# Kernel optimization log

Hardware: AMD Instinct MI355X
Metric: run time of the kernel (lower is better)

Reference implementation:

```python
import jax, jax.numpy as jnp
import numpy as np

ITERATION = 10

def setup_inputs() -> dict:
    key = jax.random.key(0)
    k1, k2, k3 = jax.random.split(key, 3)
    a_inter = jax.random.normal(k1, (8, 64, 64, 32, 32), dtype=jnp.float32)
    logits = jax.random.normal(k2, (8, 64), dtype=jnp.float32)
    W = jax.random.normal(k3, (1, 64, 64), dtype=jnp.float32)
    return {"a_inter": a_inter, "logits": logits, "W": W}


def reference(a_inter, logits, W):
    N = W.shape[1]  # num_nodes
    B = a_inter.shape[0]
    # feats: [B, N, C*H*W]
    feats = a_inter[:, :, :N, :, :].reshape(B, N, -1)
    # expand logits [B, N] -> [B, N, N] (unsqueeze(1).expand in torch)
    logits0 = jnp.broadcast_to(logits[:, None, :], (B, N, N))

    feats_norm = jnp.linalg.norm(feats, ord=2, axis=2, keepdims=True)  # [B, N, 1]
    pairwise_norm = feats_norm @ jnp.swapaxes(feats_norm, 1, 2)        # [B, N, N]
    pairwise_dot = feats @ jnp.swapaxes(feats, 1, 2)                   # [B, N, N]
    pairwise_sim = pairwise_dot / (pairwise_norm + 1e-6)
    W_sym = (W + jnp.swapaxes(W, 1, 2)) / 2.0
    pairwise_potential = pairwise_sim * W_sym                          # [B, N, N]

    unary_potential = logits0

    def body(i, l):
        probs = jnp.swapaxes(jax.nn.sigmoid(l), 1, 2)  # [B, N, N]
        # probs*pp - (1-probs)*pp == (2*probs - 1)*pp
        pp_E = jnp.sum((2.0 * probs - 1.0) * pairwise_potential, axis=2, keepdims=True)
        return unary_potential + pp_E

    logits_out = jax.lax.fori_loop(0, ITERATION, body, logits0)
    return logits_out.mean(axis=1)  # [B, N]
```

## Files before the change

### kernel.cpp

```cpp
#include <hip/hip_runtime.h>
#include <math.h>

#define BATCH 8
#define NN 64
#define DD 65536
#define BPB 64
#define NBLK (BATCH * BPB)
#define KC (DD / BPB)
#define KW (KC / 4)
#define KSTEPS (KW / 32)
#define NTRI 10
#define PSZ (NTRI * 256)

typedef float  floatx4 __attribute__((ext_vector_type(4)));
typedef __bf16 bf16x8  __attribute__((ext_vector_type(8)));

static __device__ __forceinline__ bf16x8 cvt8(float4 lo, float4 hi) {
    const unsigned sel = 0x07060302u;
    union { unsigned u[4]; bf16x8 v; } r;
    r.u[0] = __builtin_amdgcn_perm(__float_as_uint(lo.y), __float_as_uint(lo.x), sel);
    r.u[1] = __builtin_amdgcn_perm(__float_as_uint(lo.w), __float_as_uint(lo.z), sel);
    r.u[2] = __builtin_amdgcn_perm(__float_as_uint(hi.y), __float_as_uint(hi.x), sel);
    r.u[3] = __builtin_amdgcn_perm(__float_as_uint(hi.w), __float_as_uint(hi.z), sel);
    return r.v;
}

__global__ __launch_bounds__(256, 3) void gram_partial_kernel(const float* __restrict__ a,
                                                              float* __restrict__ part) {
    __shared__ __align__(16) float red[3][NTRI][64][4];

    const int bid = blockIdx.x;
    const int b = bid >> 6;
    const int c = bid & (BPB - 1);

    const int tid  = threadIdx.x;
    const int w    = tid >> 6;
    const int lane = tid & 63;
    const int m    = lane & 15;
    const int q    = lane >> 4;

    const float* base = a + (size_t)b * NN * DD + (size_t)c * KC + (size_t)w * KW
                          + (size_t)m * DD + q * 8;
    const float* p0 = base;
    const float* p1 = base + (size_t)16 * DD;
    const float* p2 = base + (size_t)32 * DD;
    const float* p3 = base + (size_t)48 * DD;

    floatx4 acc[NTRI];
    #pragma unroll
    for (int i = 0; i < NTRI; ++i) acc[i] = (floatx4)0.0f;

    float4 A0, A1, A2, A3, A4, A5, A6, A7;
    float4 B0, B1, B2, B3, B4, B5, B6, B7;

#define LOADSET(R0,R1,R2,R3,R4,R5,R6,R7, o)                                \
    R0 = *(const float4*)(p0 + (o));  R1 = *(const float4*)(p0 + (o) + 4); \
    R2 = *(const float4*)(p1 + (o));  R3 = *(const float4*)(p1 + (o) + 4); \
    R4 = *(const float4*)(p2 + (o));  R5 = *(const float4*)(p2 + (o) + 4); \
    R6 = *(const float4*)(p3 + (o));  R7 = *(const float4*)(p3 + (o) + 4);

#define MFMASET(R0,R1,R2,R3,R4,R5,R6,R7)                                   \
    {                                                                      \
        bf16x8 f0 = cvt8(R0, R1);                                          \
        bf16x8 f1 = cvt8(R2, R3);                                          \
        bf16x8 f2 = cvt8(R4, R5);                                          \
        bf16x8 f3 = cvt8(R6, R7);                                          \
        acc[0] = __builtin_amdgcn_mfma_f32_16x16x32_bf16(f0, f0, acc[0], 0, 0, 0); \
        acc[1] = __builtin_amdgcn_mfma_f32_16x16x32_bf16(f0, f1, acc[1], 0, 0, 0); \
        acc[2] = __builtin_amdgcn_mfma_f32_16x16x32_bf16(f0, f2, acc[2], 0, 0, 0); \
        acc[3] = __builtin_amdgcn_mfma_f32_16x16x32_bf16(f0, f3, acc[3], 0, 0, 0); \
        acc[4] = __builtin_amdgcn_mfma_f32_16x16x32_bf16(f1, f1, acc[4], 0, 0, 0); \
        acc[5] = __builtin_amdgcn_mfma_f32_16x16x32_bf16(f1, f2, acc[5], 0, 0, 0); \
        acc[6] = __builtin_amdgcn_mfma_f32_16x16x32_bf16(f1, f3, acc[6], 0, 0, 0); \
        acc[7] = __builtin_amdgcn_mfma_f32_16x16x32_bf16(f2, f2, acc[7], 0, 0, 0); \
        acc[8] = __builtin_amdgcn_mfma_f32_16x16x32_bf16(f2, f3, acc[8], 0, 0, 0); \
        acc[9] = __builtin_amdgcn_mfma_f32_16x16x32_bf16(f3, f3, acc[9], 0, 0, 0); \
    }

    LOADSET(A0,A1,A2,A3,A4,A5,A6,A7, 0)
    #pragma unroll
    for (int s = 0; s < KSTEPS; s += 2) {
        LOADSET(B0,B1,B2,B3,B4,B5,B6,B7, (s + 1) * 32)
        MFMASET(A0,A1,A2,A3,A4,A5,A6,A7)
        if (s + 2 < KSTEPS) { LOADSET(A0,A1,A2,A3,A4,A5,A6,A7, (s + 2) * 32) }
        MFMASET(B0,B1,B2,B3,B4,B5,B6,B7)
    }
#undef LOADSET
#undef MFMASET

    if (w > 0) {
        #pragma unroll
        for (int t = 0; t < NTRI; ++t)
            *(floatx4*)&red[w - 1][t][lane][0] = acc[t];
    }
    __syncthreads();
    if (w == 0) {
        #pragma unroll
        for (int t = 0; t < NTRI; ++t) {
            floatx4 r0 = *(const floatx4*)&red[0][t][lane][0];
            floatx4 r1 = *(const floatx4*)&red[1][t][lane][0];
            floatx4 r2 = *(const floatx4*)&red[2][t][lane][0];
            acc[t] += (r0 + r1) + r2;
        }
        float* pg = part + (size_t)bid * PSZ;
        #pragma unroll
        for (int t = 0; t < NTRI; ++t) {
            float* tp = pg + t * 256 + m;
            #pragma unroll
            for (int r = 0; r < 4; ++r)
                tp[(q * 4 + r) * 16] = acc[t][r];
        }
    }
}

__global__ __launch_bounds__(128) void gram_reduce_kernel(const float* __restrict__ part,
                                                          float* __restrict__ gram) {
    const int gid = blockIdx.x * 128 + threadIdx.x;
    const int b   = gid >> 12;
    const int idx = gid & 4095;
    const int i   = idx >> 6;
    const int j   = idx & 63;
    const int ti  = i >> 4, tj = j >> 4;
    const int ib  = ti <= tj ? ti : tj;
    const int jb  = ti <= tj ? tj : ti;
    const int slot = ib * 4 - (ib * (ib - 1)) / 2 + (jb - ib);
    const int rr  = (ti <= tj) ? (i & 15) : (j & 15);
    const int cc  = (ti <= tj) ? (j & 15) : (i & 15);
    const int off = slot * 256 + rr * 16 + cc;
    const float* p = part + (size_t)b * BPB * PSZ + off;

    float s0 = 0.f, s1 = 0.f, s2 = 0.f, s3 = 0.f;
    #pragma unroll 4
    for (int c = 0; c < BPB; c += 4) {
        s0 += p[(size_t)(c + 0) * PSZ];
        s1 += p[(size_t)(c + 1) * PSZ];
        s2 += p[(size_t)(c + 2) * PSZ];
        s3 += p[(size_t)(c + 3) * PSZ];
    }
    gram[gid] = (s0 + s1) + (s2 + s3);
}

__global__ __launch_bounds__(256) void crf_kernel(const float* __restrict__ gram,
                                                  const float* __restrict__ logits,
                                                  const float* __restrict__ Wm,
                                                  float* __restrict__ out) {
    __shared__ float pp[NN][NN + 1];
    __shared__ float E[NN];
    __shared__ float nrm[NN];
    __shared__ float part[4 * NN];

    const int b  = blockIdx.x;
    const int tid = threadIdx.x;
    const int i  = tid & 63;
    const int jq = tid >> 6;
    const float* g = gram + b * NN * NN;

    if (jq == 0) nrm[i] = sqrtf(g[i * NN + i]);
    E[i] = 0.0f;
    __syncthreads();

    const float ni = nrm[i];
    for (int jj = 0; jj < 16; ++jj) {
        int j = jq * 16 + jj;
        float wsym = 0.5f * (Wm[i * NN + j] + Wm[j * NN + i]);
        pp[i][j] = g[i * NN + j] / (ni * nrm[j] + 1e-6f) * wsym;
    }
    const float li = logits[b * NN + i];
    __syncthreads();

    for (int it = 0; it < 10; ++it) {
        float acc = 0.0f;
        for (int jj = 0; jj < 16; ++jj) {
            int j = jq * 16 + jj;
            float t = li + E[j];
            float s = 1.0f / (1.0f + expf(-t));
            acc = fmaf(2.0f * s - 1.0f, pp[i][j], acc);
        }
        part[jq * NN + i] = acc;
        __syncthreads();
        if (jq == 0)
            E[i] = part[i] + part[NN + i] + part[2 * NN + i] + part[3 * NN + i];
        __syncthreads();
    }

    if (tid < 64) {
        float s = E[tid];
        for (int off = 32; off > 0; off >>= 1) s += __shfl_down(s, off);
        float meanE = __shfl(s, 0) * (1.0f / 64.0f);
        out[b * NN + tid] = logits[b * NN + tid] + meanE;
    }
}

extern "C" void kernel_launch(void* const* d_in, const int* in_sizes, int n_in,
                              void* d_out, int out_size, void* d_ws, size_t ws_size,
                              hipStream_t stream) {
    const float* a      = (const float*)d_in[0];
    const float* logits = (const float*)d_in[1];
    const float* Wm     = (const float*)d_in[2];
    float* out  = (float*)d_out;

    float* part = (float*)d_ws;
    float* gram = part + (size_t)NBLK * PSZ;

    gram_partial_kernel<<<NBLK, 256, 0, stream>>>(a, part);
    gram_reduce_kernel<<<(BATCH * NN * NN) / 128, 128, 0, stream>>>(part, gram);
    crf_kernel<<<BATCH, 256, 0, stream>>>(gram, logits, Wm, out);
}
```

Before: 217.8 us.

## Stage bf16-converted feature chunks through double-buffered LDS for coalesced loads

The gram partial kernel now has each thread load contiguous float4s across rows, convert them to bf16 and write them into a double-buffered padded LDS tile. Each wave then reads its MFMA fragments from shared memory instead of doing strided per-lane global loads. The aim is fully coalesced global reads and an overlap of the next chunk's load with the current MFMAs. In exchange it adds LDS traffic and a block-wide barrier per chunk, and fewer loads are kept in flight per thread than in the old register-pipelined loop.

After: 225.3 us. 1.03x slower.

```diff
diff --git a/kernel.cpp b/kernel.cpp
--- a/kernel.cpp
+++ b/kernel.cpp
@@ -7,27 +7,21 @@
 #define BPB 64
 #define NBLK (BATCH * BPB)
 #define KC (DD / BPB)
-#define KW (KC / 4)
-#define KSTEPS (KW / 32)
+#define CHUNK 128
+#define NCHUNK (KC / CHUNK)
+#define LROW 144
 #define NTRI 10
 #define PSZ (NTRI * 256)
 
 typedef float  floatx4 __attribute__((ext_vector_type(4)));
 typedef __bf16 bf16x8  __attribute__((ext_vector_type(8)));
 
-static __device__ __forceinline__ bf16x8 cvt8(float4 lo, float4 hi) {
-    const unsigned sel = 0x07060302u;
-    union { unsigned u[4]; bf16x8 v; } r;
-    r.u[0] = __builtin_amdgcn_perm(__float_as_uint(lo.y), __float_as_uint(lo.x), sel);
-    r.u[1] = __builtin_amdgcn_perm(__float_as_uint(lo.w), __float_as_uint(lo.z), sel);
-    r.u[2] = __builtin_amdgcn_perm(__float_as_uint(hi.y), __float_as_uint(hi.x), sel);
-    r.u[3] = __builtin_amdgcn_perm(__float_as_uint(hi.w), __float_as_uint(hi.z), sel);
-    return r.v;
-}
-
 __global__ __launch_bounds__(256, 3) void gram_partial_kernel(const float* __restrict__ a,
                                                               float* __restrict__ part) {
-    __shared__ __align__(16) float red[3][NTRI][64][4];
+    __shared__ __align__(16) union {
+        unsigned short st[2][64 * LROW];
+        float red[3][NTRI][64][4];
+    } sh;
 
     const int bid = blockIdx.x;
     const int b = bid >> 6;
@@ -39,68 +33,72 @@
     const int m    = lane & 15;
     const int q    = lane >> 4;
 
-    const float* base = a + (size_t)b * NN * DD + (size_t)c * KC + (size_t)w * KW
-                          + (size_t)m * DD + q * 8;
-    const float* p0 = base;
-    const float* p1 = base + (size_t)16 * DD;
-    const float* p2 = base + (size_t)32 * DD;
-    const float* p3 = base + (size_t)48 * DD;
+    const int r0 = tid >> 5;
+    const int kp = tid & 31;
+    const float* gbase = a + (size_t)b * NN * DD + (size_t)c * KC
+                           + (size_t)r0 * DD + kp * 4;
+    const int lbase = r0 * LROW + kp * 4;
+
+    const unsigned sel = 0x07060302u;
 
     floatx4 acc[NTRI];
     #pragma unroll
     for (int i = 0; i < NTRI; ++i) acc[i] = (floatx4)0.0f;
 
-    float4 A0, A1, A2, A3, A4, A5, A6, A7;
-    float4 B0, B1, B2, B3, B4, B5, B6, B7;
-
-#define LOADSET(R0,R1,R2,R3,R4,R5,R6,R7, o)                                \
-    R0 = *(const float4*)(p0 + (o));  R1 = *(const float4*)(p0 + (o) + 4); \
-    R2 = *(const float4*)(p1 + (o));  R3 = *(const float4*)(p1 + (o) + 4); \
-    R4 = *(const float4*)(p2 + (o));  R5 = *(const float4*)(p2 + (o) + 4); \
-    R6 = *(const float4*)(p3 + (o));  R7 = *(const float4*)(p3 + (o) + 4);
-
-#define MFMASET(R0,R1,R2,R3,R4,R5,R6,R7)                                   \
-    {                                                                      \
-        bf16x8 f0 = cvt8(R0, R1);                                          \
-        bf16x8 f1 = cvt8(R2, R3);                                          \
-        bf16x8 f2 = cvt8(R4, R5);                                          \
-        bf16x8 f3 = cvt8(R6, R7);                                          \
-        acc[0] = __builtin_amdgcn_mfma_f32_16x16x32_bf16(f0, f0, acc[0], 0, 0, 0); \
-        acc[1] = __builtin_amdgcn_mfma_f32_16x16x32_bf16(f0, f1, acc[1], 0, 0, 0); \
-        acc[2] = __builtin_amdgcn_mfma_f32_16x16x32_bf16(f0, f2, acc[2], 0, 0, 0); \
-        acc[3] = __builtin_amdgcn_mfma_f32_16x16x32_bf16(f0, f3, acc[3], 0, 0, 0); \
-        acc[4] = __builtin_amdgcn_mfma_f32_16x16x32_bf16(f1, f1, acc[4], 0, 0, 0); \
-        acc[5] = __builtin_amdgcn_mfma_f32_16x16x32_bf16(f1, f2, acc[5], 0, 0, 0); \
-        acc[6] = __builtin_amdgcn_mfma_f32_16x16x32_bf16(f1, f3, acc[6], 0, 0, 0); \
-        acc[7] = __builtin_amdgcn_mfma_f32_16x16x32_bf16(f2, f2, acc[7], 0, 0, 0); \
-        acc[8] = __builtin_amdgcn_mfma_f32_16x16x32_bf16(f2, f3, acc[8], 0, 0, 0); \
-        acc[9] = __builtin_amdgcn_mfma_f32_16x16x32_bf16(f3, f3, acc[9], 0, 0, 0); \
-    }
-
-    LOADSET(A0,A1,A2,A3,A4,A5,A6,A7, 0)
-    #pragma unroll
-    for (int s = 0; s < KSTEPS; s += 2) {
-        LOADSET(B0,B1,B2,B3,B4,B5,B6,B7, (s + 1) * 32)
-        MFMASET(A0,A1,A2,A3,A4,A5,A6,A7)
-        if (s + 2 < KSTEPS) { LOADSET(A0,A1,A2,A3,A4,A5,A6,A7, (s + 2) * 32) }
-        MFMASET(B0,B1,B2,B3,B4,B5,B6,B7)
-    }
-#undef LOADSET
-#undef MFMASET
+    auto stage = [&](int cc, unsigned short* buf) {
+        const float* cb = gbase + cc * CHUNK;
+        float4 v[8];
+        #pragma unroll
+        for (int j = 0; j < 8; ++j)
+            v[j] = *(const float4*)(cb + (size_t)(8 * j) * DD);
+        #pragma unroll
+        for (int j = 0; j < 8; ++j) {
+            uint2 h;
+            h.x = __builtin_amdgcn_perm(__float_as_uint(v[j].y), __float_as_uint(v[j].x), sel);
+            h.y = __builtin_amdgcn_perm(__float_as_uint(v[j].w), __float_as_uint(v[j].z), sel);
+            *(uint2*)&buf[lbase + j * 8 * LROW] = h;
+        }
+    };
+
+    stage(0, sh.st[0]);
+    __syncthreads();
+
+    for (int cc = 0; cc < NCHUNK; ++cc) {
+        if (cc + 1 < NCHUNK) stage(cc + 1, sh.st[(cc + 1) & 1]);
+
+        const unsigned short* buf = sh.st[cc & 1];
+        const int fo = w * 32 + q * 8;
+        bf16x8 f0 = *(const bf16x8*)&buf[(m     ) * LROW + fo];
+        bf16x8 f1 = *(const bf16x8*)&buf[(m + 16) * LROW + fo];
+        bf16x8 f2 = *(const bf16x8*)&buf[(m + 32) * LROW + fo];
+        bf16x8 f3 = *(const bf16x8*)&buf[(m + 48) * LROW + fo];
+        acc[0] = __builtin_amdgcn_mfma_f32_16x16x32_bf16(f0, f0, acc[0], 0, 0, 0);
+        acc[1] = __builtin_amdgcn_mfma_f32_16x16x32_bf16(f0, f1, acc[1], 0, 0, 0);
+        acc[2] = __builtin_amdgcn_mfma_f32_16x16x32_bf16(f0, f2, acc[2], 0, 0, 0);
+        acc[3] = __builtin_amdgcn_mfma_f32_16x16x32_bf16(f0, f3, acc[3], 0, 0, 0);
+        acc[4] = __builtin_amdgcn_mfma_f32_16x16x32_bf16(f1, f1, acc[4], 0, 0, 0);
+        acc[5] = __builtin_amdgcn_mfma_f32_16x16x32_bf16(f1, f2, acc[5], 0, 0, 0);
+        acc[6] = __builtin_amdgcn_mfma_f32_16x16x32_bf16(f1, f3, acc[6], 0, 0, 0);
+        acc[7] = __builtin_amdgcn_mfma_f32_16x16x32_bf16(f2, f2, acc[7], 0, 0, 0);
+        acc[8] = __builtin_amdgcn_mfma_f32_16x16x32_bf16(f2, f3, acc[8], 0, 0, 0);
+        acc[9] = __builtin_amdgcn_mfma_f32_16x16x32_bf16(f3, f3, acc[9], 0, 0, 0);
+
+        __syncthreads();
+    }
 
     if (w > 0) {
         #pragma unroll
         for (int t = 0; t < NTRI; ++t)
-            *(floatx4*)&red[w - 1][t][lane][0] = acc[t];
+            *(floatx4*)&sh.red[w - 1][t][lane][0] = acc[t];
     }
     __syncthreads();
     if (w == 0) {
         #pragma unroll
         for (int t = 0; t < NTRI; ++t) {
-            floatx4 r0 = *(const floatx4*)&red[0][t][lane][0];
-            floatx4 r1 = *(const floatx4*)&red[1][t][lane][0];
-            floatx4 r2 = *(const floatx4*)&red[2][t][lane][0];
-            acc[t] += (r0 + r1) + r2;
+            floatx4 x0 = *(const floatx4*)&sh.red[0][t][lane][0];
+            floatx4 x1 = *(const floatx4*)&sh.red[1][t][lane][0];
+            floatx4 x2 = *(const floatx4*)&sh.red[2][t][lane][0];
+            acc[t] += (x0 + x1) + x2;
         }
         float* pg = part + (size_t)bid * PSZ;
         #pragma unroll
```
